# Kernel tuning notes

Measured on AMD Instinct MI355X. Metric: run time of the kernel, lower is better.

Reference implementation:

```python
import jax, jax.numpy as jnp
import numpy as np

INPUT_SIZE = 1
HIDDEN = 30
B, T = 8192, 512


def setup_inputs() -> dict:
    key = jax.random.key(0)
    ks = jax.random.split(key, 7)
    s_ih = 1.0 / np.sqrt(HIDDEN)
    batch = jax.random.normal(ks[0], (B, T, INPUT_SIZE), dtype=jnp.float32)
    # PyTorch LSTM params: gate order i, f, g, o stacked along first dim (4H)
    W_ih = jax.random.uniform(ks[1], (4 * HIDDEN, INPUT_SIZE), minval=-s_ih, maxval=s_ih, dtype=jnp.float32)
    W_hh = jax.random.uniform(ks[2], (4 * HIDDEN, HIDDEN), minval=-s_ih, maxval=s_ih, dtype=jnp.float32)
    b_ih = jax.random.uniform(ks[3], (4 * HIDDEN,), minval=-s_ih, maxval=s_ih, dtype=jnp.float32)
    b_hh = jax.random.uniform(ks[4], (4 * HIDDEN,), minval=-s_ih, maxval=s_ih, dtype=jnp.float32)
    W_fc = jax.random.uniform(ks[5], (1, HIDDEN), minval=-s_ih, maxval=s_ih, dtype=jnp.float32)
    b_fc = jax.random.uniform(ks[6], (1,), minval=-s_ih, maxval=s_ih, dtype=jnp.float32)
    return {"batch": batch, "W_ih": W_ih, "W_hh": W_hh, "b_ih": b_ih, "b_hh": b_hh, "W_fc": W_fc, "b_fc": b_fc}


def _lstm_final_h(x, W_ih, W_hh, b_ih, b_hh):
    # x: [B, T, I] -> final hidden state h_T: [B, H]
    Bx = x.shape[0]
    H = W_hh.shape[1]
    # Precompute input-side gate projections for all timesteps: [T, B, 4H]
    xg = jnp.einsum('bti,gi->tbg', x, W_ih) + (b_ih + b_hh)

    def step(carry, xt):
        h, c = carry
        gates = xt + h @ W_hh.T  # [B, 4H]
        i, f, g, o = jnp.split(gates, 4, axis=-1)
        i = jax.nn.sigmoid(i)
        f = jax.nn.sigmoid(f)
        g = jnp.tanh(g)
        o = jax.nn.sigmoid(o)
        c = f * c + i * g
        h = o * jnp.tanh(c)
        return (h, c), None

    h0 = jnp.zeros((Bx, H), dtype=x.dtype)
    c0 = jnp.zeros((Bx, H), dtype=x.dtype)
    (hT, _), _ = jax.lax.scan(step, (h0, c0), xg)
    return hT


def reference(batch, W_ih, W_hh, b_ih, b_hh, W_fc, b_fc):
    hT = _lstm_final_h(batch, W_ih, W_hh, b_ih, b_hh)  # [B, H]
    out = hT @ W_fc.T + b_fc  # [B, 1]
    return out.squeeze(-1)  # [B]
```

## Files before the change

### kernel.cpp

```cpp
#include <hip/hip_runtime.h>

#define HID 30
#define TS  512
#define NB  16
#define LOG2E 1.44269504088896340736f
#define XSTR 17
#define HI   20

typedef __attribute__((ext_vector_type(8))) short bf16x8;
typedef __attribute__((ext_vector_type(4))) float f32x4;

__device__ __forceinline__ float rcp_f(float x){ return __builtin_amdgcn_rcpf(x); }
__device__ __forceinline__ float ex2_f(float x){ return __builtin_amdgcn_exp2f(x); }

__global__ __launch_bounds__(256, 2)
void lstm_mfma_u2(const float* __restrict__ batch,
                  const float* __restrict__ W_ih,
                  const float* __restrict__ W_hh,
                  const float* __restrict__ b_ih,
                  const float* __restrict__ b_hh,
                  const float* __restrict__ W_fc,
                  const float* __restrict__ b_fc,
                  float* __restrict__ out)
{
    __shared__ float xs[TS * XSTR];
    __shared__ int   hhi[2][NB][HI];
    __shared__ int   hlo[2][NB][HI];

    const int tid  = threadIdx.x;
    const int w    = tid >> 6;
    const int lane = tid & 63;
    const int q    = lane >> 4;
    const int col  = lane & 15;
    const int b0   = blockIdx.x * NB;

    for (int i = 0; i < 32; ++i) {
        const int flat = i * 256 + tid;
        const int e = flat >> 9, tt = flat & 511;
        xs[tt * XSTR + e] = batch[(size_t)(b0 + e) * TS + tt];
    }
    for (int i = tid; i < NB * HI; i += 256) {
        (&hhi[0][0][0])[i] = 0;
        (&hlo[0][0][0])[i] = 0;
    }

    bf16x8 ahi[2], alo[2];
    #pragma unroll
    for (int tau = 0; tau < 2; ++tau) {
        const int gate = col & 3;
        const int unit = 8 * w + 2 * (col >> 2) + tau;
        const float sG = (gate == 2) ? (-2.0f * LOG2E) : (-LOG2E);
        const int R = gate * HID + unit;
        #pragma unroll
        for (int jj = 0; jj < 8; ++jj) {
            const int kk = q * 8 + jj;
            float wv = 0.0f;
            if (unit < HID) {
                if (kk < HID)      wv = W_hh[R * HID + kk];
                else if (kk == 30) wv = b_ih[R] + b_hh[R];
                else               wv = W_ih[R];
            }
            wv *= sG;
            const __bf16 hi = (__bf16)wv;
            const __bf16 lo = (__bf16)(wv - (float)hi);
            ahi[tau][jj] = (short)__builtin_bit_cast(unsigned short, hi);
            alo[tau][jj] = (short)__builtin_bit_cast(unsigned short, lo);
        }
    }

    __syncthreads();

    const float TWOL = 2.0f * LOG2E;
    float cm0 = 0.0f, cm1 = 0.0f;

#define STEP(T, RB, WB)                                                        \
{                                                                              \
        \
    int4 vhi = *(const int4*)&hhi[RB][col][4 * q];                             \
    int4 vlo = *(const int4*)&hlo[RB][col][4 * q];                             \
    const float xv = xs[(T) * XSTR + col];                                     \
    {                                                                          \
        const __bf16 xh = (__bf16)xv;                                          \
        const __bf16 xl = (__bf16)(xv - (float)xh);                            \
        const unsigned xhb = __builtin_bit_cast(unsigned short, xh);           \
        const unsigned xlb = __builtin_bit_cast(unsigned short, xl);           \
        vhi.w = (q == 3) ? (int)(0x3F80u | (xhb << 16)) : vhi.w;               \
        vlo.w = (q == 3) ? (int)(xlb << 16)             : vlo.w;               \
    }                                                                          \
    const bf16x8 bhi = __builtin_bit_cast(bf16x8, vhi);                        \
    const bf16x8 blo = __builtin_bit_cast(bf16x8, vlo);                        \
    f32x4 a0 = {0.f, 0.f, 0.f, 0.f}, a1 = {0.f, 0.f, 0.f, 0.f};               \
    a0 = __builtin_amdgcn_mfma_f32_16x16x32_bf16(ahi[0], bhi, a0, 0, 0, 0);    \
    a1 = __builtin_amdgcn_mfma_f32_16x16x32_bf16(ahi[1], bhi, a1, 0, 0, 0);    \
    a0 = __builtin_amdgcn_mfma_f32_16x16x32_bf16(ahi[0], blo, a0, 0, 0, 0);    \
    a1 = __builtin_amdgcn_mfma_f32_16x16x32_bf16(ahi[1], blo, a1, 0, 0, 0);    \
    a0 = __builtin_amdgcn_mfma_f32_16x16x32_bf16(alo[0], bhi, a0, 0, 0, 0);    \
    a1 = __builtin_amdgcn_mfma_f32_16x16x32_bf16(alo[1], bhi, a1, 0, 0, 0);    \
        \
    float h0, h1;                                                              \
    {                                                                          \
        const float ei = ex2_f(a0[0]), ef = ex2_f(a0[1]);                      \
        const float eg = ex2_f(a0[2]), eo = ex2_f(a0[3]);                      \
        const float t1 = 1.0f + ei, t2 = 1.0f + eg;                            \
        const float P = t1 * t2, Q = 1.0f + ef;                                \
        const float m1 = (t2 - 2.0f) * Q;                                      \
        const float num = fmaf(TWOL, m1, cm0 * P);                             \
        cm0 = num * rcp_f(P * Q);                                              \
        const float e = ex2_f(cm0);                                            \
        h0 = (1.0f - e) * rcp_f((1.0f + e) * (1.0f + eo));                     \
    }                                                                          \
    {                                                                          \
        const float ei = ex2_f(a1[0]), ef = ex2_f(a1[1]);                      \
        const float eg = ex2_f(a1[2]), eo = ex2_f(a1[3]);                      \
        const float t1 = 1.0f + ei, t2 = 1.0f + eg;                            \
        const float P = t1 * t2, Q = 1.0f + ef;                                \
        const float m1 = (t2 - 2.0f) * Q;                                      \
        const float num = fmaf(TWOL, m1, cm1 * P);                             \
        cm1 = num * rcp_f(P * Q);                                              \
        const float e = ex2_f(cm1);                                            \
        h1 = (1.0f - e) * rcp_f((1.0f + e) * (1.0f + eo));                     \
    }                                                                          \
            \
    {                                                                          \
        const __bf16 h0h = (__bf16)h0;                                         \
        const __bf16 h0l = (__bf16)(h0 - (float)h0h);                          \
        const __bf16 h1h = (__bf16)h1;                                         \
        const __bf16 h1l = (__bf16)(h1 - (float)h1h);                          \
        hhi[WB][col][4 * w + q] =                                              \
            (int)((unsigned)__builtin_bit_cast(unsigned short, h0h) |          \
                 ((unsigned)__builtin_bit_cast(unsigned short, h1h) << 16));   \
        hlo[WB][col][4 * w + q] =                                              \
            (int)((unsigned)__builtin_bit_cast(unsigned short, h0l) |          \
                 ((unsigned)__builtin_bit_cast(unsigned short, h1l) << 16));   \
    }                                                                          \
    __syncthreads();                                                           \
}

    for (int t2 = 0; t2 < TS / 2; ++t2) {
        STEP(2 * t2,     0, 1)
        STEP(2 * t2 + 1, 1, 0)
    }
#undef STEP

    if (tid < NB) {
        const short* hh = (const short*)&hhi[0][tid][0];
        const short* hl = (const short*)&hlo[0][tid][0];
        float acc = b_fc[0];
        #pragma unroll
        for (int u = 0; u < HID; ++u) {
            const float hv =
                (float)__builtin_bit_cast(__bf16, (unsigned short)hh[u]) +
                (float)__builtin_bit_cast(__bf16, (unsigned short)hl[u]);
            acc = fmaf(hv, W_fc[u], acc);
        }
        out[b0 + tid] = acc;
    }
}

extern "C" void kernel_launch(void* const* d_in, const int* in_sizes, int n_in,
                              void* d_out, int out_size, void* d_ws, size_t ws_size,
                              hipStream_t stream) {
    const float* batch = (const float*)d_in[0];
    const float* W_ih  = (const float*)d_in[1];
    const float* W_hh  = (const float*)d_in[2];
    const float* b_ih  = (const float*)d_in[3];
    const float* b_hh  = (const float*)d_in[4];
    const float* W_fc  = (const float*)d_in[5];
    const float* b_fc  = (const float*)d_in[6];
    float* out = (float*)d_out;

    const int blocks = 8192 / NB;
    lstm_mfma_u2<<<blocks, 256, 0, stream>>>(batch, W_ih, W_hh, b_ih, b_hh,
                                             W_fc, b_fc, out);
}
```

Measured before the change: 212.6 us.

## Split hidden units across 8 waves with one MFMA tile per wave

Doubles the block to 512 threads so each wave handles a single 16-row gate tile (4 units) instead of two. This halves the per-wave MFMA and activation chain on the serial recurrence. Hidden state is now stored as shorts, and the input is pre-split into packed bf16 hi/lo words during loading, which removes that split from the per-step path. The cost is a barrier across 8 waves every step and more threads per block competing for occupancy.

```diff
diff --git a/kernel.cpp b/kernel.cpp
--- a/kernel.cpp
+++ b/kernel.cpp
@@ -5,7 +5,7 @@
 #define NB  16
 #define LOG2E 1.44269504088896340736f
 #define XSTR 17
-#define HI   20
+#define HS   40
 
 typedef __attribute__((ext_vector_type(8))) short bf16x8;
 typedef __attribute__((ext_vector_type(4))) float f32x4;
@@ -13,8 +13,8 @@
 __device__ __forceinline__ float rcp_f(float x){ return __builtin_amdgcn_rcpf(x); }
 __device__ __forceinline__ float ex2_f(float x){ return __builtin_amdgcn_exp2f(x); }
 
-__global__ __launch_bounds__(256, 2)
-void lstm_mfma_u2(const float* __restrict__ batch,
+__global__ __launch_bounds__(512, 4)
+void lstm_mfma_u1(const float* __restrict__ batch,
                   const float* __restrict__ W_ih,
                   const float* __restrict__ W_hh,
                   const float* __restrict__ b_ih,
@@ -23,9 +23,9 @@
                   const float* __restrict__ b_fc,
                   float* __restrict__ out)
 {
-    __shared__ float xs[TS * XSTR];
-    __shared__ int   hhi[2][NB][HI];
-    __shared__ int   hlo[2][NB][HI];
+    __shared__ int xs[TS * XSTR];
+    __shared__ __align__(16) short hhi[2][NB][HS];
+    __shared__ __align__(16) short hlo[2][NB][HS];
 
     const int tid  = threadIdx.x;
     const int w    = tid >> 6;
@@ -34,21 +34,24 @@
     const int col  = lane & 15;
     const int b0   = blockIdx.x * NB;
 
-    for (int i = 0; i < 32; ++i) {
-        const int flat = i * 256 + tid;
-        const int e = flat >> 9, tt = flat & 511;
-        xs[tt * XSTR + e] = batch[(size_t)(b0 + e) * TS + tt];
+    #pragma unroll 4
+    for (int i = 0; i < NB; ++i) {
+        const float v = batch[(size_t)(b0 + i) * TS + tid];
+        const __bf16 xh = (__bf16)v;
+        const __bf16 xl = (__bf16)(v - (float)xh);
+        xs[tid * XSTR + i] =
+            (int)((unsigned)__builtin_bit_cast(unsigned short, xh) |
+                 ((unsigned)__builtin_bit_cast(unsigned short, xl) << 16));
     }
-    for (int i = tid; i < NB * HI; i += 256) {
-        (&hhi[0][0][0])[i] = 0;
-        (&hlo[0][0][0])[i] = 0;
+    for (int i = tid; i < 2 * NB * HS / 2; i += 512) {
+        ((int*)hhi)[i] = 0;
+        ((int*)hlo)[i] = 0;
     }
 
-    bf16x8 ahi[2], alo[2];
-    #pragma unroll
-    for (int tau = 0; tau < 2; ++tau) {
+    bf16x8 ahi, alo;
+    {
         const int gate = col & 3;
-        const int unit = 8 * w + 2 * (col >> 2) + tau;
+        const int unit = 4 * w + (col >> 2);
         const float sG = (gate == 2) ? (-2.0f * LOG2E) : (-LOG2E);
         const int R = gate * HID + unit;
         #pragma unroll
@@ -63,76 +66,43 @@
             wv *= sG;
             const __bf16 hi = (__bf16)wv;
             const __bf16 lo = (__bf16)(wv - (float)hi);
-            ahi[tau][jj] = (short)__builtin_bit_cast(unsigned short, hi);
-            alo[tau][jj] = (short)__builtin_bit_cast(unsigned short, lo);
+            ahi[jj] = (short)__builtin_bit_cast(unsigned short, hi);
+            alo[jj] = (short)__builtin_bit_cast(unsigned short, lo);
         }
     }
 
     __syncthreads();
 
     const float TWOL = 2.0f * LOG2E;
-    float cm0 = 0.0f, cm1 = 0.0f;
+    float cm = 0.0f;
 
 #define STEP(T, RB, WB)                                                        \
 {                                                                              \
-        \
-    int4 vhi = *(const int4*)&hhi[RB][col][4 * q];                             \
-    int4 vlo = *(const int4*)&hlo[RB][col][4 * q];                             \
-    const float xv = xs[(T) * XSTR + col];                                     \
-    {                                                                          \
-        const __bf16 xh = (__bf16)xv;                                          \
-        const __bf16 xl = (__bf16)(xv - (float)xh);                            \
-        const unsigned xhb = __builtin_bit_cast(unsigned short, xh);           \
-        const unsigned xlb = __builtin_bit_cast(unsigned short, xl);           \
-        vhi.w = (q == 3) ? (int)(0x3F80u | (xhb << 16)) : vhi.w;               \
-        vlo.w = (q == 3) ? (int)(xlb << 16)             : vlo.w;               \
-    }                                                                          \
+    int4 vhi = *(const int4*)&hhi[RB][col][8 * q];                             \
+    int4 vlo = *(const int4*)&hlo[RB][col][8 * q];                             \
+    const unsigned xp = (unsigned)xs[(T) * XSTR + col];                        \
+    vhi.w = (q == 3) ? (int)(0x3F80u | (xp << 16)) : vhi.w;                    \
+    vlo.w = (q == 3) ? (int)(xp & 0xFFFF0000u)     : vlo.w;                    \
     const bf16x8 bhi = __builtin_bit_cast(bf16x8, vhi);                        \
     const bf16x8 blo = __builtin_bit_cast(bf16x8, vlo);                        \
-    f32x4 a0 = {0.f, 0.f, 0.f, 0.f}, a1 = {0.f, 0.f, 0.f, 0.f};               \
-    a0 = __builtin_amdgcn_mfma_f32_16x16x32_bf16(ahi[0], bhi, a0, 0, 0, 0);    \
-    a1 = __builtin_amdgcn_mfma_f32_16x16x32_bf16(ahi[1], bhi, a1, 0, 0, 0);    \
-    a0 = __builtin_amdgcn_mfma_f32_16x16x32_bf16(ahi[0], blo, a0, 0, 0, 0);    \
-    a1 = __builtin_amdgcn_mfma_f32_16x16x32_bf16(ahi[1], blo, a1, 0, 0, 0);    \
-    a0 = __builtin_amdgcn_mfma_f32_16x16x32_bf16(alo[0], bhi, a0, 0, 0, 0);    \
-    a1 = __builtin_amdgcn_mfma_f32_16x16x32_bf16(alo[1], bhi, a1, 0, 0, 0);    \
-        \
-    float h0, h1;                                                              \
-    {                                                                          \
-        const float ei = ex2_f(a0[0]), ef = ex2_f(a0[1]);                      \
-        const float eg = ex2_f(a0[2]), eo = ex2_f(a0[3]);                      \
-        const float t1 = 1.0f + ei, t2 = 1.0f + eg;                            \
-        const float P = t1 * t2, Q = 1.0f + ef;                                \
-        const float m1 = (t2 - 2.0f) * Q;                                      \
-        const float num = fmaf(TWOL, m1, cm0 * P);                             \
-        cm0 = num * rcp_f(P * Q);                                              \
-        const float e = ex2_f(cm0);                                            \
-        h0 = (1.0f - e) * rcp_f((1.0f + e) * (1.0f + eo));                     \
-    }                                                                          \
-    {                                                                          \
-        const float ei = ex2_f(a1[0]), ef = ex2_f(a1[1]);                      \
-        const float eg = ex2_f(a1[2]), eo = ex2_f(a1[3]);                      \
-        const float t1 = 1.0f + ei, t2 = 1.0f + eg;                            \
-        const float P = t1 * t2, Q = 1.0f + ef;                                \
-        const float m1 = (t2 - 2.0f) * Q;                                      \
-        const float num = fmaf(TWOL, m1, cm1 * P);                             \
-        cm1 = num * rcp_f(P * Q);                                              \
-        const float e = ex2_f(cm1);                                            \
-        h1 = (1.0f - e) * rcp_f((1.0f + e) * (1.0f + eo));                     \
-    }                                                                          \
-            \
-    {                                                                          \
-        const __bf16 h0h = (__bf16)h0;                                         \
-        const __bf16 h0l = (__bf16)(h0 - (float)h0h);                          \
-        const __bf16 h1h = (__bf16)h1;                                         \
-        const __bf16 h1l = (__bf16)(h1 - (float)h1h);                          \
-        hhi[WB][col][4 * w + q] =                                              \
-            (int)((unsigned)__builtin_bit_cast(unsigned short, h0h) |          \
-                 ((unsigned)__builtin_bit_cast(unsigned short, h1h) << 16));   \
-        hlo[WB][col][4 * w + q] =                                              \
-            (int)((unsigned)__builtin_bit_cast(unsigned short, h0l) |          \
-                 ((unsigned)__builtin_bit_cast(unsigned short, h1l) << 16));   \
-    }                                                                          \
+    f32x4 a = {0.f, 0.f, 0.f, 0.f};                                            \
+    a = __builtin_amdgcn_mfma_f32_16x16x32_bf16(ahi, bhi, a, 0, 0, 0);         \
+    a = __builtin_amdgcn_mfma_f32_16x16x32_bf16(ahi, blo, a, 0, 0, 0);         \
+    a = __builtin_amdgcn_mfma_f32_16x16x32_bf16(alo, bhi, a, 0, 0, 0);         \
+                             \
+    const float ei = ex2_f(a[0]), ef = ex2_f(a[1]);                            \
+    const float eg = ex2_f(a[2]), eo = ex2_f(a[3]);                            \
+    const float P  = (1.0f + ei) * (1.0f + eg);                                \
+    const float Q  = 1.0f + ef;                                                \
+    const float m1 = (eg - 1.0f) * Q;                                          \
+    const float num = fmaf(TWOL, m1, cm * P);                                  \
+    cm = num * rcp_f(P * Q);                                                   \
+    const float e = ex2_f(cm);                                                 \
+    const float h = (1.0f - e) * rcp_f((1.0f + e) * (1.0f + eo));              \
+    const __bf16 hh = (__bf16)h;                                               \
+    const __bf16 hl = (__bf16)(h - (float)hh);                                 \
+    hhi[WB][col][4 * w + q] = (short)__builtin_bit_cast(unsigned short, hh);   \
+    hlo[WB][col][4 * w + q] = (short)__builtin_bit_cast(unsigned short, hl);   \
     __syncthreads();                                                           \
 }
 
@@ -143,8 +113,8 @@
 #undef STEP
 
     if (tid < NB) {
-        const short* hh = (const short*)&hhi[0][tid][0];
-        const short* hl = (const short*)&hlo[0][tid][0];
+        const short* hh = &hhi[0][tid][0];
+        const short* hl = &hlo[0][tid][0];
         float acc = b_fc[0];
         #pragma unroll
         for (int u = 0; u < HID; ++u) {
@@ -170,6 +140,6 @@
     float* out = (float*)d_out;
 
     const int blocks = 8192 / NB;
-    lstm_mfma_u2<<<blocks, 256, 0, stream>>>(batch, W_ih, W_hh, b_ih, b_hh,
+    lstm_mfma_u1<<<blocks, 512, 0, stream>>>(batch, W_ih, W_hh, b_ih, b_hh,
                                              W_fc, b_fc, out);
 }
```

Measured after the change: 186.9 us (median of 2 runs). 12.1% less time.
